# Kernel optimization log

Measured on AMD Instinct MI355X. Metric: run time of the kernel, lower is better.

## Reference

```python
import jax, jax.numpy as jnp
import numpy as np

B, N, F, E = 2, 50000, 128, 500000


def setup_inputs() -> dict:
    key = jax.random.key(0)
    ks = jax.random.split(key, 7)
    x0 = jax.random.normal(ks[0], (B, N, F), dtype=jnp.float32)
    dst = jax.random.randint(ks[1], (E,), 0, N, dtype=jnp.int32)
    src = jax.random.randint(ks[2], (E,), 0, N, dtype=jnp.int32)
    # torch Linear weights: [out_features, in_features]
    w0 = jax.random.normal(ks[3], (F, 2 * F), dtype=jnp.float32) * 0.05
    b0 = jax.random.normal(ks[4], (F,), dtype=jnp.float32) * 0.05
    w1 = jax.random.normal(ks[5], (F, F), dtype=jnp.float32) * 0.05
    b1 = jax.random.normal(ks[6], (F,), dtype=jnp.float32) * 0.05
    return {"x0": x0, "dst": dst, "src": src, "w0": w0, "b0": b0, "w1": w1, "b1": b1}


def reference(x0, dst, src, w0, b0, w1, b1):
    n = x0.shape[1]
    # gather source node features per edge: [B, E, F] -> [E, B, F] for segment ops
    xe = jnp.transpose(x0[:, src], (1, 0, 2))
    # scatter-reduce over destination nodes (include_self=False semantics)
    s = jax.ops.segment_sum(xe, dst, num_segments=n)                      # [N, B, F]
    mx = jax.ops.segment_max(xe, dst, num_segments=n)                     # [N, B, F]
    cnt = jax.ops.segment_sum(jnp.ones((dst.shape[0],), x0.dtype), dst, num_segments=n)  # [N]
    has_edge = (cnt > 0)[:, None, None]
    x0t = jnp.transpose(x0, (1, 0, 2))                                    # [N, B, F]
    # nodes with no incoming edges keep their original values
    mean = jnp.where(has_edge, s / jnp.maximum(cnt, 1.0)[:, None, None], x0t)
    amax = jnp.where(has_edge, mx, x0t)
    x = jnp.concatenate([mean, amax], axis=-1)                            # [N, B, 2F]
    h = jax.nn.relu(jnp.einsum('nbf,of->nbo', x, w0) + b0)
    # dropout is identity in eval mode
    out = x0t + jnp.einsum('nbf,of->nbo', h, w1) + b1
    return jnp.transpose(out, (1, 0, 2))                                  # [B, N, F]
```

## Files before the change

kernel.cpp:

```cpp
#include <hip/hip_runtime.h>

#define NN 50000
#define FF 128
constexpr int NBF2 = NN * 256;
constexpr int CAP  = 64;
constexpr int CSTR = 16;

typedef __attribute__((ext_vector_type(4))) short short4v;
typedef __attribute__((ext_vector_type(8))) short short8;
typedef __attribute__((ext_vector_type(4))) float floatx4;

__device__ __forceinline__ unsigned short f2bf(float x) {
    unsigned int u = __float_as_uint(x);
    unsigned int r = (u + 0x7fff + ((u >> 16) & 1)) >> 16;
    return (unsigned short)r;
}
__device__ __forceinline__ float bf2f(short x) {
    return __uint_as_float(((unsigned int)(unsigned short)x) << 16);
}

__global__ __launch_bounds__(256)
void convert_fill(const int* __restrict__ dst, const int* __restrict__ src, int E,
                  const float* __restrict__ x0,
                  const float* __restrict__ w0, const float* __restrict__ w1,
                  int* __restrict__ cursor, unsigned short* __restrict__ esrc,
                  unsigned short* __restrict__ x0b,
                  unsigned short* __restrict__ w0b, unsigned short* __restrict__ w1b) {
    int i = blockIdx.x * 256 + threadIdx.x;
    if (i < E) {
        int d = dst[i];
        int pos = atomicAdd(&cursor[d * CSTR], 1);
        if (pos < CAP) esrc[d * CAP + pos] = (unsigned short)src[i];
    }
    int stride = gridDim.x * 256;
    for (int p = i; p < NBF2 / 4; p += stride) {
        int v0 = p * 4;
        int n = v0 >> 8;
        int b = (v0 >> 7) & 1;
        int f = v0 & 127;
        floatx4 in = __builtin_nontemporal_load((const floatx4*)&x0[(b * NN + n) * FF + f]);
        short4v o = { (short)f2bf(in.x), (short)f2bf(in.y), (short)f2bf(in.z), (short)f2bf(in.w) };
        *(short4v*)&x0b[v0] = o;
    }
    if (i < 128 * 256) w0b[i] = f2bf(w0[i]);
    if (i < 128 * 128) w1b[i] = f2bf(w1[i]);
}

constexpr int NPB = 8;
constexpr int XCP = 256 + 8;
constexpr int HSP = 128 + 8;

__global__ __launch_bounds__(256, 8)
void fused_gcn(const unsigned short* __restrict__ x0b,
               const float* __restrict__ x0,
               const int* __restrict__ deg,
               const unsigned short* __restrict__ esrc,
               const unsigned short* __restrict__ w0b,
               const float* __restrict__ b0,
               const unsigned short* __restrict__ w1b,
               const float* __restrict__ b1,
               float* __restrict__ out) {
    __shared__ unsigned short xc[16 * XCP];
    __shared__ unsigned short hs[16 * HSP];

    int t = threadIdx.x;
    int q = t >> 6;
    int l = t & 63;
    int n0 = blockIdx.x * NPB;
    int nA = n0 + q * 2;
    int nB = nA + 1;

    bool hi = (l >= 32);
    int fo8 = (l & 31) * 8;
    const float NEG_INF = __int_as_float(0xFF800000);

    int vA = esrc[nA * CAP + l];
    int vB = esrc[nB * CAP + l];
    int dA = min(__builtin_amdgcn_readfirstlane(deg[nA * CSTR]), CAP);
    int dB = min(__builtin_amdgcn_readfirstlane(deg[nB * CSTR]), CAP);

#define ACC8(r) { \
    float v0=bf2f(r[0]), v1=bf2f(r[1]), v2=bf2f(r[2]), v3=bf2f(r[3]); \
    float v4=bf2f(r[4]), v5=bf2f(r[5]), v6=bf2f(r[6]), v7=bf2f(r[7]); \
    S0+=v0;S1+=v1;S2+=v2;S3+=v3;S4+=v4;S5+=v5;S6+=v6;S7+=v7; \
    M0=fmaxf(M0,v0);M1=fmaxf(M1,v1);M2=fmaxf(M2,v2);M3=fmaxf(M3,v3); \
    M4=fmaxf(M4,v4);M5=fmaxf(M5,v5);M6=fmaxf(M6,v6);M7=fmaxf(M7,v7); }

#define PAIR_LOAD(vv, k, rname) \
    int ue##rname = __builtin_amdgcn_readlane(vv, (k));     ue##rname = (ue##rname < NN) ? ue##rname : 0; \
    int uo##rname = __builtin_amdgcn_readlane(vv, (k) + 1); uo##rname = (uo##rname < NN) ? uo##rname : 0; \
    int us##rname = hi ? uo##rname : ue##rname; \
    short8 rname = *(const short8*)&x0b[(us##rname << 8) + fo8];

#define GATHER_NODE(vv, dd, nn, g) { \
    float S0=0,S1=0,S2=0,S3=0,S4=0,S5=0,S6=0,S7=0; \
    float M0=NEG_INF,M1=NEG_INF,M2=NEG_INF,M3=NEG_INF; \
    float M4=NEG_INF,M5=NEG_INF,M6=NEG_INF,M7=NEG_INF; \
    int kk = 0; \
    for (; kk + 7 < dd; kk += 8) {           \
        PAIR_LOAD(vv, kk,     ra) PAIR_LOAD(vv, kk + 2, rb) \
        PAIR_LOAD(vv, kk + 4, rc) PAIR_LOAD(vv, kk + 6, rd) \
        ACC8(ra) ACC8(rb) ACC8(rc) ACC8(rd) \
    } \
    if (kk + 3 < dd) { \
        PAIR_LOAD(vv, kk, ra) PAIR_LOAD(vv, kk + 2, rb) \
        ACC8(ra) ACC8(rb) \
        kk += 4; \
    } \
    if (kk + 1 < dd) { \
        PAIR_LOAD(vv, kk, ra) \
        ACC8(ra) \
        kk += 2; \
    } \
    if (dd & 1) {                             \
        int ut = __builtin_amdgcn_readlane(vv, dd - 1); ut = (ut < NN) ? ut : 0; \
        short8 rt = *(const short8*)&x0b[(ut << 8) + fo8]; \
        if (!hi) { ACC8(rt) } \
    } \
     \
    { float o; \
      o=__shfl_xor(S0,32); S0+=o; o=__shfl_xor(S1,32); S1+=o; \
      o=__shfl_xor(S2,32); S2+=o; o=__shfl_xor(S3,32); S3+=o; \
      o=__shfl_xor(S4,32); S4+=o; o=__shfl_xor(S5,32); S5+=o; \
      o=__shfl_xor(S6,32); S6+=o; o=__shfl_xor(S7,32); S7+=o; \
      o=__shfl_xor(M0,32); M0=fmaxf(M0,o); o=__shfl_xor(M1,32); M1=fmaxf(M1,o); \
      o=__shfl_xor(M2,32); M2=fmaxf(M2,o); o=__shfl_xor(M3,32); M3=fmaxf(M3,o); \
      o=__shfl_xor(M4,32); M4=fmaxf(M4,o); o=__shfl_xor(M5,32); M5=fmaxf(M5,o); \
      o=__shfl_xor(M6,32); M6=fmaxf(M6,o); o=__shfl_xor(M7,32); M7=fmaxf(M7,o); } \
    if (!hi) { \
        float e0,e1,e2,e3,e4,e5,e6,e7, a0,a1,a2,a3,a4,a5,a6,a7; \
        if (dd > 0) { \
            float inv = 1.0f / (float)dd; \
            e0=S0*inv;e1=S1*inv;e2=S2*inv;e3=S3*inv;e4=S4*inv;e5=S5*inv;e6=S6*inv;e7=S7*inv; \
            a0=M0;a1=M1;a2=M2;a3=M3;a4=M4;a5=M5;a6=M6;a7=M7; \
        } else { \
            short8 rr = *(const short8*)&x0b[((nn) << 8) + fo8]; \
            e0=a0=bf2f(rr[0]); e1=a1=bf2f(rr[1]); e2=a2=bf2f(rr[2]); e3=a3=bf2f(rr[3]); \
            e4=a4=bf2f(rr[4]); e5=a5=bf2f(rr[5]); e6=a6=bf2f(rr[6]); e7=a7=bf2f(rr[7]); \
        } \
        int row = (q * 2 + g) * 2 + (l >> 4);       \
        int fb  = (l & 15) * 8; \
        short8 mv = { (short)f2bf(e0),(short)f2bf(e1),(short)f2bf(e2),(short)f2bf(e3), \
                      (short)f2bf(e4),(short)f2bf(e5),(short)f2bf(e6),(short)f2bf(e7) }; \
        short8 av = { (short)f2bf(a0),(short)f2bf(a1),(short)f2bf(a2),(short)f2bf(a3), \
                      (short)f2bf(a4),(short)f2bf(a5),(short)f2bf(a6),(short)f2bf(a7) }; \
        *(short8*)&xc[row * XCP + fb]       = mv; \
        *(short8*)&xc[row * XCP + 128 + fb] = av; \
    } \
}

    GATHER_NODE(vA, dA, nA, 0)
    GATHER_NODE(vB, dB, nB, 1)
#undef GATHER_NODE
#undef PAIR_LOAD
#undef ACC8
    __syncthreads();

    int m    = l & 15;
    int quad = l >> 4;
    int colbase = q * 32;

    floatx4 acc[2];
#pragma unroll
    for (int ct = 0; ct < 2; ++ct) acc[ct] = (floatx4){0.f, 0.f, 0.f, 0.f};
#pragma unroll
    for (int ks = 0; ks < 8; ++ks) {
        short8 a = *(const short8*)&xc[m * XCP + ks * 32 + quad * 8];
#pragma unroll
        for (int ct = 0; ct < 2; ++ct) {
            short8 bfr = *(const short8*)&w0b[(colbase + ct * 16 + m) * 256 + ks * 32 + quad * 8];
            acc[ct] = __builtin_amdgcn_mfma_f32_16x16x32_bf16(a, bfr, acc[ct], 0, 0, 0);
        }
    }
#pragma unroll
    for (int ct = 0; ct < 2; ++ct) {
        int col = colbase + ct * 16 + m;
        float bias = b0[col];
#pragma unroll
        for (int r = 0; r < 4; ++r) {
            int row = quad * 4 + r;
            hs[row * HSP + col] = f2bf(fmaxf(acc[ct][r] + bias, 0.0f));
        }
    }
    __syncthreads();

    floatx4 acc2[2];
#pragma unroll
    for (int ct = 0; ct < 2; ++ct) acc2[ct] = (floatx4){0.f, 0.f, 0.f, 0.f};
#pragma unroll
    for (int ks = 0; ks < 4; ++ks) {
        short8 a = *(const short8*)&hs[m * HSP + ks * 32 + quad * 8];
#pragma unroll
        for (int ct = 0; ct < 2; ++ct) {
            short8 bfr = *(const short8*)&w1b[(colbase + ct * 16 + m) * 128 + ks * 32 + quad * 8];
            acc2[ct] = __builtin_amdgcn_mfma_f32_16x16x32_bf16(a, bfr, acc2[ct], 0, 0, 0);
        }
    }
#pragma unroll
    for (int ct = 0; ct < 2; ++ct) {
        int col = colbase + ct * 16 + m;
        float bias = b1[col];
#pragma unroll
        for (int r = 0; r < 4; ++r) {
            int row = quad * 4 + r;
            int n  = n0 + (row >> 1);
            int b2 = row & 1;
            int oi = (b2 * NN + n) * FF + col;
            float xv = __builtin_nontemporal_load(&x0[oi]);
            __builtin_nontemporal_store(xv + bias + acc2[ct][r], &out[oi]);
        }
    }
}

extern "C" void kernel_launch(void* const* d_in, const int* in_sizes, int n_in,
                              void* d_out, int out_size, void* d_ws, size_t ws_size,
                              hipStream_t stream) {
    const float* x0  = (const float*)d_in[0];
    const int*   dst = (const int*)d_in[1];
    const int*   src = (const int*)d_in[2];
    const float* w0  = (const float*)d_in[3];
    const float* b0  = (const float*)d_in[4];
    const float* w1  = (const float*)d_in[5];
    const float* b1  = (const float*)d_in[6];
    float* out = (float*)d_out;
    int E = in_sizes[1];

    int* cursor = (int*)d_ws;
    unsigned short* esrc = (unsigned short*)(cursor + (size_t)NN * CSTR);
    unsigned short* x0b  = esrc + (size_t)NN * CAP;
    unsigned short* w0b  = x0b + NBF2;
    unsigned short* w1b  = w0b + 128 * 256;

    int eb = (E + 255) / 256;

    hipMemsetAsync(cursor, 0, (size_t)NN * CSTR * sizeof(int), stream);
    convert_fill<<<eb, 256, 0, stream>>>(dst, src, E, x0, w0, w1, cursor, esrc, x0b, w0b, w1b);
    fused_gcn<<<NN / NPB, 256, 0, stream>>>(x0b, x0, cursor, esrc, w0b, b0, w1b, b1, out);
}
```

Before: 236.4 us.

## Merge per-wave two-node gathers into one edge stream and read residual from bf16

New measurement: 303.1 us. +28.2%, slower.

```diff
diff --git a/kernel.cpp b/kernel.cpp
--- a/kernel.cpp
+++ b/kernel.cpp
@@ -5,6 +5,9 @@
 constexpr int NBF2 = NN * 256;
 constexpr int CAP  = 64;
 constexpr int CSTR = 16;
+constexpr int NPB  = 8;
+constexpr int XCP = 256 + 8;
+constexpr int HSP = 128 + 8;
 
 typedef __attribute__((ext_vector_type(4))) short short4v;
 typedef __attribute__((ext_vector_type(8))) short short8;
@@ -46,13 +49,8 @@
     if (i < 128 * 128) w1b[i] = f2bf(w1[i]);
 }
 
-constexpr int NPB = 8;
-constexpr int XCP = 256 + 8;
-constexpr int HSP = 128 + 8;
-
-__global__ __launch_bounds__(256, 8)
+__global__ __launch_bounds__(256, 6)
 void fused_gcn(const unsigned short* __restrict__ x0b,
-               const float* __restrict__ x0,
                const int* __restrict__ deg,
                const unsigned short* __restrict__ esrc,
                const unsigned short* __restrict__ w0b,
@@ -78,59 +76,92 @@
     int vB = esrc[nB * CAP + l];
     int dA = min(__builtin_amdgcn_readfirstlane(deg[nA * CSTR]), CAP);
     int dB = min(__builtin_amdgcn_readfirstlane(deg[nB * CSTR]), CAP);
-
-#define ACC8(r) { \
-    float v0=bf2f(r[0]), v1=bf2f(r[1]), v2=bf2f(r[2]), v3=bf2f(r[3]); \
-    float v4=bf2f(r[4]), v5=bf2f(r[5]), v6=bf2f(r[6]), v7=bf2f(r[7]); \
-    S0+=v0;S1+=v1;S2+=v2;S3+=v3;S4+=v4;S5+=v5;S6+=v6;S7+=v7; \
-    M0=fmaxf(M0,v0);M1=fmaxf(M1,v1);M2=fmaxf(M2,v2);M3=fmaxf(M3,v3); \
-    M4=fmaxf(M4,v4);M5=fmaxf(M5,v5);M6=fmaxf(M6,v6);M7=fmaxf(M7,v7); }
-
-#define PAIR_LOAD(vv, k, rname) \
-    int ue##rname = __builtin_amdgcn_readlane(vv, (k));     ue##rname = (ue##rname < NN) ? ue##rname : 0; \
-    int uo##rname = __builtin_amdgcn_readlane(vv, (k) + 1); uo##rname = (uo##rname < NN) ? uo##rname : 0; \
+    int dT = dA + dB;
+
+    float SA0=0,SA1=0,SA2=0,SA3=0,SA4=0,SA5=0,SA6=0,SA7=0;
+    float SB0=0,SB1=0,SB2=0,SB3=0,SB4=0,SB5=0,SB6=0,SB7=0;
+    float MA0=NEG_INF,MA1=NEG_INF,MA2=NEG_INF,MA3=NEG_INF;
+    float MA4=NEG_INF,MA5=NEG_INF,MA6=NEG_INF,MA7=NEG_INF;
+    float MB0=NEG_INF,MB1=NEG_INF,MB2=NEG_INF,MB3=NEG_INF;
+    float MB4=NEG_INF,MB5=NEG_INF,MB6=NEG_INF,MB7=NEG_INF;
+
+#define SRCLANE(e) ( (e) < dA ? __builtin_amdgcn_readlane(vA, (e)) \
+                              : __builtin_amdgcn_readlane(vB, (e) - dA) )
+
+#define ACC8A(r) { \
+    float v0=bf2f(r[0]),v1=bf2f(r[1]),v2=bf2f(r[2]),v3=bf2f(r[3]); \
+    float v4=bf2f(r[4]),v5=bf2f(r[5]),v6=bf2f(r[6]),v7=bf2f(r[7]); \
+    SA0+=v0;SA1+=v1;SA2+=v2;SA3+=v3;SA4+=v4;SA5+=v5;SA6+=v6;SA7+=v7; \
+    MA0=fmaxf(MA0,v0);MA1=fmaxf(MA1,v1);MA2=fmaxf(MA2,v2);MA3=fmaxf(MA3,v3); \
+    MA4=fmaxf(MA4,v4);MA5=fmaxf(MA5,v5);MA6=fmaxf(MA6,v6);MA7=fmaxf(MA7,v7); }
+
+#define ACC8B(r) { \
+    float v0=bf2f(r[0]),v1=bf2f(r[1]),v2=bf2f(r[2]),v3=bf2f(r[3]); \
+    float v4=bf2f(r[4]),v5=bf2f(r[5]),v6=bf2f(r[6]),v7=bf2f(r[7]); \
+    SB0+=v0;SB1+=v1;SB2+=v2;SB3+=v3;SB4+=v4;SB5+=v5;SB6+=v6;SB7+=v7; \
+    MB0=fmaxf(MB0,v0);MB1=fmaxf(MB1,v1);MB2=fmaxf(MB2,v2);MB3=fmaxf(MB3,v3); \
+    MB4=fmaxf(MB4,v4);MB5=fmaxf(MB5,v5);MB6=fmaxf(MB6,v6);MB7=fmaxf(MB7,v7); }
+
+#define PAIR_LOAD(e, rname) \
+    int ue##rname = SRCLANE(e); \
+    int uo##rname = SRCLANE((e) + 1); \
     int us##rname = hi ? uo##rname : ue##rname; \
     short8 rname = *(const short8*)&x0b[(us##rname << 8) + fo8];
 
-#define GATHER_NODE(vv, dd, nn, g) { \
-    float S0=0,S1=0,S2=0,S3=0,S4=0,S5=0,S6=0,S7=0; \
-    float M0=NEG_INF,M1=NEG_INF,M2=NEG_INF,M3=NEG_INF; \
-    float M4=NEG_INF,M5=NEG_INF,M6=NEG_INF,M7=NEG_INF; \
-    int kk = 0; \
-    for (; kk + 7 < dd; kk += 8) {           \
-        PAIR_LOAD(vv, kk,     ra) PAIR_LOAD(vv, kk + 2, rb) \
-        PAIR_LOAD(vv, kk + 4, rc) PAIR_LOAD(vv, kk + 6, rd) \
-        ACC8(ra) ACC8(rb) ACC8(rc) ACC8(rd) \
-    } \
-    if (kk + 3 < dd) { \
-        PAIR_LOAD(vv, kk, ra) PAIR_LOAD(vv, kk + 2, rb) \
-        ACC8(ra) ACC8(rb) \
-        kk += 4; \
-    } \
-    if (kk + 1 < dd) { \
-        PAIR_LOAD(vv, kk, ra) \
-        ACC8(ra) \
-        kk += 2; \
-    } \
-    if (dd & 1) {                             \
-        int ut = __builtin_amdgcn_readlane(vv, dd - 1); ut = (ut < NN) ? ut : 0; \
-        short8 rt = *(const short8*)&x0b[(ut << 8) + fo8]; \
-        if (!hi) { ACC8(rt) } \
-    } \
-     \
-    { float o; \
-      o=__shfl_xor(S0,32); S0+=o; o=__shfl_xor(S1,32); S1+=o; \
-      o=__shfl_xor(S2,32); S2+=o; o=__shfl_xor(S3,32); S3+=o; \
-      o=__shfl_xor(S4,32); S4+=o; o=__shfl_xor(S5,32); S5+=o; \
-      o=__shfl_xor(S6,32); S6+=o; o=__shfl_xor(S7,32); S7+=o; \
-      o=__shfl_xor(M0,32); M0=fmaxf(M0,o); o=__shfl_xor(M1,32); M1=fmaxf(M1,o); \
-      o=__shfl_xor(M2,32); M2=fmaxf(M2,o); o=__shfl_xor(M3,32); M3=fmaxf(M3,o); \
-      o=__shfl_xor(M4,32); M4=fmaxf(M4,o); o=__shfl_xor(M5,32); M5=fmaxf(M5,o); \
-      o=__shfl_xor(M6,32); M6=fmaxf(M6,o); o=__shfl_xor(M7,32); M7=fmaxf(M7,o); } \
+#define ACC_PAIR(e, rname) { \
+    if ((e) + 1 < dA)      { ACC8A(rname) } \
+    else if ((e) >= dA)    { ACC8B(rname) } \
+    else { if (!hi) { ACC8A(rname) } else { ACC8B(rname) } } }
+
+    int kk = 0;
+    for (; kk + 11 < dT; kk += 12) {
+        PAIR_LOAD(kk + 0,  ra) PAIR_LOAD(kk + 2,  rb) PAIR_LOAD(kk + 4,  rc)
+        PAIR_LOAD(kk + 6,  rd) PAIR_LOAD(kk + 8,  re) PAIR_LOAD(kk + 10, rf)
+        ACC_PAIR(kk + 0,  ra) ACC_PAIR(kk + 2,  rb) ACC_PAIR(kk + 4,  rc)
+        ACC_PAIR(kk + 6,  rd) ACC_PAIR(kk + 8,  re) ACC_PAIR(kk + 10, rf)
+    }
+    for (; kk + 3 < dT; kk += 4) {
+        PAIR_LOAD(kk, ra) PAIR_LOAD(kk + 2, rb)
+        ACC_PAIR(kk, ra) ACC_PAIR(kk + 2, rb)
+    }
+    if (kk + 1 < dT) {
+        PAIR_LOAD(kk, ra)
+        ACC_PAIR(kk, ra)
+        kk += 2;
+    }
+    if (kk < dT) {
+        int ut = SRCLANE(dT - 1);
+        short8 rt = *(const short8*)&x0b[(ut << 8) + fo8];
+        if (dT - 1 < dA) { if (!hi) { ACC8A(rt) } }
+        else             { if (!hi) { ACC8B(rt) } }
+    }
+#undef ACC_PAIR
+#undef PAIR_LOAD
+#undef SRCLANE
+
+    { float o;
+      o=__shfl_xor(SA0,32); SA0+=o; o=__shfl_xor(SA1,32); SA1+=o;
+      o=__shfl_xor(SA2,32); SA2+=o; o=__shfl_xor(SA3,32); SA3+=o;
+      o=__shfl_xor(SA4,32); SA4+=o; o=__shfl_xor(SA5,32); SA5+=o;
+      o=__shfl_xor(SA6,32); SA6+=o; o=__shfl_xor(SA7,32); SA7+=o;
+      o=__shfl_xor(MA0,32); MA0=fmaxf(MA0,o); o=__shfl_xor(MA1,32); MA1=fmaxf(MA1,o);
+      o=__shfl_xor(MA2,32); MA2=fmaxf(MA2,o); o=__shfl_xor(MA3,32); MA3=fmaxf(MA3,o);
+      o=__shfl_xor(MA4,32); MA4=fmaxf(MA4,o); o=__shfl_xor(MA5,32); MA5=fmaxf(MA5,o);
+      o=__shfl_xor(MA6,32); MA6=fmaxf(MA6,o); o=__shfl_xor(MA7,32); MA7=fmaxf(MA7,o);
+      o=__shfl_xor(SB0,32); SB0+=o; o=__shfl_xor(SB1,32); SB1+=o;
+      o=__shfl_xor(SB2,32); SB2+=o; o=__shfl_xor(SB3,32); SB3+=o;
+      o=__shfl_xor(SB4,32); SB4+=o; o=__shfl_xor(SB5,32); SB5+=o;
+      o=__shfl_xor(SB6,32); SB6+=o; o=__shfl_xor(SB7,32); SB7+=o;
+      o=__shfl_xor(MB0,32); MB0=fmaxf(MB0,o); o=__shfl_xor(MB1,32); MB1=fmaxf(MB1,o);
+      o=__shfl_xor(MB2,32); MB2=fmaxf(MB2,o); o=__shfl_xor(MB3,32); MB3=fmaxf(MB3,o);
+      o=__shfl_xor(MB4,32); MB4=fmaxf(MB4,o); o=__shfl_xor(MB5,32); MB5=fmaxf(MB5,o);
+      o=__shfl_xor(MB6,32); MB6=fmaxf(MB6,o); o=__shfl_xor(MB7,32); MB7=fmaxf(MB7,o); }
+
+#define FINAL_N(g, nn, dgx, S0,S1,S2,S3,S4,S5,S6,S7, M0,M1,M2,M3,M4,M5,M6,M7) \
     if (!hi) { \
         float e0,e1,e2,e3,e4,e5,e6,e7, a0,a1,a2,a3,a4,a5,a6,a7; \
-        if (dd > 0) { \
-            float inv = 1.0f / (float)dd; \
+        if (dgx > 0) { \
+            float inv = 1.0f / (float)dgx; \
             e0=S0*inv;e1=S1*inv;e2=S2*inv;e3=S3*inv;e4=S4*inv;e5=S5*inv;e6=S6*inv;e7=S7*inv; \
             a0=M0;a1=M1;a2=M2;a3=M3;a4=M4;a5=M5;a6=M6;a7=M7; \
         } else { \
@@ -138,7 +169,7 @@
             e0=a0=bf2f(rr[0]); e1=a1=bf2f(rr[1]); e2=a2=bf2f(rr[2]); e3=a3=bf2f(rr[3]); \
             e4=a4=bf2f(rr[4]); e5=a5=bf2f(rr[5]); e6=a6=bf2f(rr[6]); e7=a7=bf2f(rr[7]); \
         } \
-        int row = (q * 2 + g) * 2 + (l >> 4);       \
+        int row = (q * 2 + (g)) * 2 + (l >> 4); \
         int fb  = (l & 15) * 8; \
         short8 mv = { (short)f2bf(e0),(short)f2bf(e1),(short)f2bf(e2),(short)f2bf(e3), \
                       (short)f2bf(e4),(short)f2bf(e5),(short)f2bf(e6),(short)f2bf(e7) }; \
@@ -146,14 +177,12 @@
                       (short)f2bf(a4),(short)f2bf(a5),(short)f2bf(a6),(short)f2bf(a7) }; \
         *(short8*)&xc[row * XCP + fb]       = mv; \
         *(short8*)&xc[row * XCP + 128 + fb] = av; \
-    } \
-}
-
-    GATHER_NODE(vA, dA, nA, 0)
-    GATHER_NODE(vB, dB, nB, 1)
-#undef GATHER_NODE
-#undef PAIR_LOAD
-#undef ACC8
+    }
+    FINAL_N(0, nA, dA, SA0,SA1,SA2,SA3,SA4,SA5,SA6,SA7, MA0,MA1,MA2,MA3,MA4,MA5,MA6,MA7)
+    FINAL_N(1, nB, dB, SB0,SB1,SB2,SB3,SB4,SB5,SB6,SB7, MB0,MB1,MB2,MB3,MB4,MB5,MB6,MB7)
+#undef FINAL_N
+#undef ACC8A
+#undef ACC8B
     __syncthreads();
 
     int m    = l & 15;
@@ -205,9 +234,8 @@
             int row = quad * 4 + r;
             int n  = n0 + (row >> 1);
             int b2 = row & 1;
-            int oi = (b2 * NN + n) * FF + col;
-            float xv = __builtin_nontemporal_load(&x0[oi]);
-            __builtin_nontemporal_store(xv + bias + acc2[ct][r], &out[oi]);
+            float xv = bf2f((short)x0b[(n << 8) + (b2 << 7) + col]);
+            out[(b2 * NN + n) * FF + col] = xv + bias + acc2[ct][r];
         }
     }
 }
@@ -233,7 +261,7 @@
 
     int eb = (E + 255) / 256;
 
-    hipMemsetAsync(cursor, 0, (size_t)NN * CSTR * sizeof(int), stream);
+    (void)hipMemsetAsync(cursor, 0, (size_t)NN * CSTR * sizeof(int), stream);
     convert_fill<<<eb, 256, 0, stream>>>(dst, src, E, x0, w0, w1, cursor, esrc, x0b, w0b, w1b);
-    fused_gcn<<<NN / NPB, 256, 0, stream>>>(x0b, x0, cursor, esrc, w0b, b0, w1b, b1, out);
-}
+    fused_gcn<<<NN / NPB, 256, 0, stream>>>(x0b, cursor, esrc, w0b, b0, w1b, b1, out);
+}
```
